# Performance work log

Measured on AMD Instinct MI355X. Metric: run time of the kernel, lower is better.

Reference implementation:

```python
import jax, jax.numpy as jnp
import numpy as np

VOCAB, EMB, NDIM, B, T = 50000, 300, 512, 128, 128


def gru_cell(x, h, Wih, Whh, bih, bhh):
    # torch nn.GRU gate order: [r, z, n]
    gi = x @ Wih.T + bih
    gh = h @ Whh.T + bhh
    i_r, i_z, i_n = jnp.split(gi, 3, axis=-1)
    h_r, h_z, h_n = jnp.split(gh, 3, axis=-1)
    r = jax.nn.sigmoid(i_r + h_r)
    z = jax.nn.sigmoid(i_z + h_z)
    n = jnp.tanh(i_n + r * h_n)
    return (1.0 - z) * n + z * h


def masked_gru(X, mask, h0, Wih, Whh, bih, bhh):
    # X: T x B x d, mask: T x B, h0: B x n. Replicates _gru_forward:
    # step-0 output is stored UNmasked (o_tm1 is None), later steps blend.
    h_raw = gru_cell(X[0], h0, Wih, Whh, bih, bhh)
    m0 = mask[0][:, None]
    h = h_raw * m0 + h0 * (1.0 - m0)
    o = h_raw

    def step(carry, inp):
        h, o = carry
        x_t, m_t = inp
        m = m_t[:, None]
        hr = gru_cell(x_t, h, Wih, Whh, bih, bhh)
        h_new = hr * m + h * (1.0 - m)
        o_new = hr * m + o * (1.0 - m)
        return (h_new, o_new), o_new

    (h_f, _), o_rest = jax.lax.scan(step, (h, o), (X[1:], mask[1:]))
    return jnp.concatenate([o[None], o_rest], axis=0), h_f


def rte_forward(premise, hypothesis, E, p_Wih, p_Whh, p_bih, p_bhh,
                h_Wih, h_Whh, h_bih, h_bhh, m_Wih, m_Whh, m_bih, m_bhh,
                W_y, W_h, W_r, W_alpha, out_W, out_b):
    bsz = premise.shape[0]
    n_dim = W_y.shape[0]
    mask_p = (premise != 0).astype(E.dtype).T            # T x B
    mask_h = (hypothesis != 0).astype(E.dtype).T
    enc_p = E[premise].transpose(1, 0, 2)                # T x B x EMB (eval: no dropout)
    enc_h = E[hypothesis].transpose(1, 0, 2)
    h0 = jnp.zeros((bsz, n_dim), dtype=E.dtype)
    o_p, h_n = masked_gru(enc_p, mask_p, h0, p_Wih, p_Whh, p_bih, p_bhh)
    o_h, _ = masked_gru(enc_h, mask_h, h_n, h_Wih, h_Whh, h_bih, h_bhh)

    Y = o_p.transpose(1, 0, 2)                           # B x Tp x n
    Yw = Y @ W_y                                         # hoisted: constant across steps
    maskY = mask_p.T                                     # B x Tp

    def step(r, inp):
        h_t, m_t = inp
        s = h_t @ W_h + r @ W_r                          # B x n
        M = jnp.tanh(Yw + s[:, None, :])                 # B x Tp x n
        alpha = (M @ W_alpha)[..., 0]                    # B x Tp
        alpha = alpha - 1000.0 * (1.0 - maskY)
        alpha = jax.nn.softmax(alpha, axis=-1)
        a = jnp.einsum('bt,btn->bn', alpha, Y)
        m_in = jnp.concatenate([a, h_t], axis=-1)        # B x 2n
        rr = gru_cell(m_in, r, m_Wih, m_Whh, m_bih, m_bhh)
        m = m_t[:, None]
        r_new = rr * m + r * (1.0 - m)
        return r_new, alpha

    r0 = jnp.zeros((bsz, n_dim), dtype=E.dtype)
    r_f, _alpha_vec = jax.lax.scan(step, r0, (o_h, mask_h))
    logits = r_f @ out_W.T + out_b                       # B x 3
    return jax.nn.log_softmax(logits, axis=-1)


def setup_inputs():
    key = jax.random.key(0)
    ks = jax.random.split(key, 22)
    s = 0.05
    def rn(k, sh):
        return jax.random.normal(k, sh, dtype=jnp.float32) * s
    G = 3 * NDIM
    return {
        "premise": jax.random.randint(ks[0], (B, T), 0, VOCAB),
        "hypothesis": jax.random.randint(ks[1], (B, T), 0, VOCAB),
        "E": rn(ks[2], (VOCAB, EMB)),
        "p_Wih": rn(ks[3], (G, EMB)), "p_Whh": rn(ks[4], (G, NDIM)),
        "p_bih": rn(ks[5], (G,)), "p_bhh": rn(ks[6], (G,)),
        "h_Wih": rn(ks[7], (G, EMB)), "h_Whh": rn(ks[8], (G, NDIM)),
        "h_bih": rn(ks[9], (G,)), "h_bhh": rn(ks[10], (G,)),
        "m_Wih": rn(ks[11], (G, 2 * NDIM)), "m_Whh": rn(ks[12], (G, NDIM)),
        "m_bih": rn(ks[13], (G,)), "m_bhh": rn(ks[14], (G,)),
        "W_y": rn(ks[15], (NDIM, NDIM)), "W_h": rn(ks[16], (NDIM, NDIM)),
        "W_r": rn(ks[17], (NDIM, NDIM)), "W_alpha": rn(ks[18], (NDIM, 1)),
        "out_W": rn(ks[19], (3, NDIM)), "out_b": rn(ks[20], (3,)),
    }


def reference(premise, hypothesis, E, p_Wih, p_Whh, p_bih, p_bhh,
              h_Wih, h_Whh, h_bih, h_bhh, m_Wih, m_Whh, m_bih, m_bhh,
              W_y, W_h, W_r, W_alpha, out_W, out_b):
    return rte_forward(premise, hypothesis, E, p_Wih, p_Whh, p_bih, p_bhh,
                       h_Wih, h_Whh, h_bih, h_bhh, m_Wih, m_Whh, m_bih, m_bhh,
                       W_y, W_h, W_r, W_alpha, out_W, out_b)
```

## Files before the change

kernel.cpp:

```cpp
#include <hip/hip_runtime.h>
#include <math.h>

#define B_SZ 128
#define T_SZ 128
#define EMBD 300
#define ND 512
#define G3 1536
#define FPAD 32
#define NFID 128
#define NREP 8

typedef short s16x8 __attribute__((ext_vector_type(8)));
typedef float f32x4 __attribute__((ext_vector_type(4)));
typedef unsigned long long u64;

__device__ __forceinline__ unsigned short f2b(float x) {
    unsigned u = __float_as_uint(x);
    unsigned r = (u + 0x7fff + ((u >> 16) & 1)) >> 16;
    return (unsigned short)r;
}
__device__ __forceinline__ float b2f(unsigned short v) {
    return __uint_as_float(((unsigned)v) << 16);
}
__device__ __forceinline__ unsigned pk2(float lo, float hi) {
    return (unsigned)f2b(lo) | ((unsigned)f2b(hi) << 16);
}
__device__ __forceinline__ float fsigmoid(float x) { return 1.0f / (1.0f + __expf(-x)); }
__device__ __forceinline__ float ftanh(float x) { return 1.0f - 2.0f / (__expf(2.0f * x) + 1.0f); }

__device__ __forceinline__ float dot2bf(unsigned a, unsigned b, float c) {
    asm("v_dot2_f32_bf16 %0, %1, %2, %0" : "+v"(c) : "v"(a), "v"(b));
    return c;
}

__device__ __forceinline__ f32x4 mfma16(s16x8 a, s16x8 b, f32x4 c) {
    return __builtin_amdgcn_mfma_f32_16x16x32_bf16(a, b, c, 0, 0, 0);
}

__device__ __forceinline__ u64 cld64(const void* p) {
    return __hip_atomic_load((const u64*)p, __ATOMIC_RELAXED, __HIP_MEMORY_SCOPE_AGENT);
}
__device__ __forceinline__ void cst64(void* p, u64 v) {
    __hip_atomic_store((u64*)p, v, __ATOMIC_RELAXED, __HIP_MEMORY_SCOPE_AGENT);
}
__device__ __forceinline__ unsigned cld32(const void* p) {
    return __hip_atomic_load((const unsigned*)p, __ATOMIC_RELAXED, __HIP_MEMORY_SCOPE_AGENT);
}
__device__ __forceinline__ void cst32(void* p, unsigned v) {
    __hip_atomic_store((unsigned*)p, v, __ATOMIC_RELAXED, __HIP_MEMORY_SCOPE_AGENT);
}
__device__ __forceinline__ s16x8 cld_frag(const unsigned short* p) {
    union { u64 q[2]; s16x8 v; } u;
    u.q[0] = cld64(p);
    u.q[1] = cld64(p + 4);
    return u.v;
}

__device__ __forceinline__ void postflag(unsigned* flags, int base, int id, unsigned ep)
{
    if (threadIdx.x < NREP)
        cst32(&flags[((long)threadIdx.x * NFID + base + id) * FPAD], ep);
}
__device__ __forceinline__ void waitflags(const unsigned* flags, int base, int n,
                                          unsigned ep, int rep)
{
    const unsigned* fr = flags + (long)rep * NFID * FPAD;
    if (threadIdx.x < 64) {
#pragma unroll 1
        for (int i = threadIdx.x; i < n; i += 64)
            while (cld32(&fr[(long)(base + i) * FPAD]) < ep)
                __builtin_amdgcn_s_sleep(2);
    }
    __syncthreads();
}
__device__ __forceinline__ void fbar(unsigned* flags, int base, int nb, unsigned ep)
{
    __syncthreads();
    postflag(flags, base, blockIdx.x & 63, ep);
    waitflags(flags, base, nb, ep, blockIdx.x & 7);
}

#define FB_GRUP 0
#define FB_GRUH 64

template<typename AT, bool OB>
__global__ __launch_bounds__(256)
void mfma_gemm(const AT* __restrict__ A, const int* __restrict__ idxA,
               const unsigned short* __restrict__ Wb, const float* __restrict__ bias,
               void* __restrict__ Cv,
               int M, int N, int K, int ldA, int Kpad, int ldC)
{
    __shared__ unsigned short As[64][40];
    __shared__ unsigned short Bs[64][40];
    const int tid = threadIdx.x;
    const int wv = tid >> 6, lane = tid & 63;
    const int wm = wv >> 1, wn = wv & 1;
    const int m0 = blockIdx.y * 64, n0 = blockIdx.x * 64;

    f32x4 acc[2][2] = {{{0.f,0.f,0.f,0.f},{0.f,0.f,0.f,0.f}},
                       {{0.f,0.f,0.f,0.f},{0.f,0.f,0.f,0.f}}};
    const int r_st = tid >> 2, k_st = (tid & 3) * 8;

    long arow = -1;
    {
        int gm = m0 + r_st;
        if (gm < M) arow = idxA ? (long)idxA[gm] : (long)gm;
    }

    const int kIters = (K + 31) / 32;
    for (int it = 0; it < kIters; ++it) {
        const int kg = it * 32 + k_st;
        {
            s16x8 pk = {0,0,0,0,0,0,0,0};
            if (arow >= 0) {
                if constexpr (sizeof(AT) == 2) {
                    if (kg + 8 <= K) {
                        pk = *(const s16x8*)((const unsigned short*)A + arow * (long)ldA + kg);
                    } else {
#pragma unroll
                        for (int j = 0; j < 8; ++j)
                            if (kg + j < K) pk[j] = (short)((const unsigned short*)A)[arow * (long)ldA + kg + j];
                    }
                } else {
                    if (kg + 8 <= K) {
                        const float* p = (const float*)A + arow * (long)ldA + kg;
                        f32x4 u0 = *(const f32x4*)p;
                        f32x4 u1 = *(const f32x4*)(p + 4);
#pragma unroll
                        for (int j = 0; j < 4; ++j) { pk[j] = (short)f2b(u0[j]); pk[4+j] = (short)f2b(u1[j]); }
                    } else {
#pragma unroll
                        for (int j = 0; j < 8; ++j) {
                            int kk = kg + j;
                            if (kk < K) pk[j] = (short)f2b(((const float*)A)[arow * (long)ldA + kk]);
                        }
                    }
                }
            }
            *(s16x8*)&As[r_st][k_st] = pk;
        }
        {
            int gn = n0 + r_st;
            s16x8 pk = {0,0,0,0,0,0,0,0};
            if (gn < N) pk = *(const s16x8*)&Wb[(long)gn * Kpad + kg];
            *(s16x8*)&Bs[r_st][k_st] = pk;
        }
        __syncthreads();
        {
            const int koff = (lane >> 4) * 8;
            s16x8 af[2], bfr[2];
#pragma unroll
            for (int f = 0; f < 2; ++f) {
                af[f]  = *(s16x8*)&As[wm * 32 + f * 16 + (lane & 15)][koff];
                bfr[f] = *(s16x8*)&Bs[wn * 32 + f * 16 + (lane & 15)][koff];
            }
#pragma unroll
            for (int fi = 0; fi < 2; ++fi)
#pragma unroll
                for (int fj = 0; fj < 2; ++fj)
                    acc[fi][fj] = mfma16(af[fi], bfr[fj], acc[fi][fj]);
        }
        __syncthreads();
    }
#pragma unroll
    for (int fi = 0; fi < 2; ++fi)
#pragma unroll
        for (int fj = 0; fj < 2; ++fj)
#pragma unroll
            for (int r = 0; r < 4; ++r) {
                int m = m0 + wm * 32 + fi * 16 + (lane >> 4) * 4 + r;
                int n = n0 + wn * 32 + fj * 16 + (lane & 15);
                if (m < M && n < N) {
                    float v = acc[fi][fj][r];
                    if (bias) v += bias[n];
                    if constexpr (OB) ((unsigned short*)Cv)[(long)m * ldC + n] = f2b(v);
                    else               ((float*)Cv)[(long)m * ldC + n] = v;
                }
            }
}

#define GRU_NB 64
__global__ __launch_bounds__(256, 1)
void gru_chain(const unsigned short* __restrict__ Whh_b, const float* __restrict__ GI,
               const float* __restrict__ bhh, const int* __restrict__ toks,
               float* __restrict__ h32,
               unsigned short* __restrict__ h16a, unsigned short* __restrict__ h16b,
               unsigned short* __restrict__ o_bt,
               unsigned* __restrict__ flags, int fbase)
{
    __shared__ unsigned short wlds[3][16][512];
    __shared__ unsigned short ht[64][20];
    const int tid = threadIdx.x;
    const int wv = tid >> 6, lane = tid & 63;
    const int dt = blockIdx.x & 31, bh = blockIdx.x >> 5;
    const int b0 = bh * 64;

    for (int s = 0; s < 12; ++s) {
        int slot = tid + s * 256;
        int g = slot >> 10, rem = slot & 1023, ks = rem >> 6, ln = rem & 63;
        int row = g * ND + dt * 16 + (ln & 15);
        int k = ks * 32 + (ln >> 4) * 8;
        *(s16x8*)&wlds[g][ks][ln * 8] = *(const s16x8*)&Whh_b[(long)row * ND + k];
    }
    __syncthreads();

    const int d = dt * 16 + (lane & 15);
    const int brow = b0 + wv * 16 + (lane >> 4) * 4;
    const long fhrd = ((long)(bh * 4 + wv) * 16) << 9;

    const int bl = tid & 63, dq = tid >> 6;
    const long fhwr = (((long)(bh * 4 + (bl >> 4)) * 16 + (dt >> 1)) << 9)
                    + (((((dt & 1) * 16 + dq * 4) >> 3) * 16 + (bl & 15)) * 8)
                    + (((dt & 1) * 16 + dq * 4) & 7);

    float hreg[4];
#pragma unroll
    for (int rr = 0; rr < 4; ++rr) hreg[rr] = h32[(long)(brow + rr) * ND + d];

    float o_run[4] = {0.f, 0.f, 0.f, 0.f};
    unsigned ep = 0;

    for (int t = 0; t < T_SZ; ++t) {
        const unsigned short* hin16 = (t & 1) ? h16b : h16a;
        unsigned short* hout16 = (t & 1) ? h16a : h16b;

        const float* git = GI + (long)t * (B_SZ * G3);
        float gi_r[4], gi_z[4], gi_n[4]; int mk[4];
#pragma unroll
        for (int rr = 0; rr < 4; ++rr) {
            int b = brow + rr;
            gi_r[rr] = git[(long)b * G3 + d];
            gi_z[rr] = git[(long)b * G3 + ND + d];
            gi_n[rr] = git[(long)b * G3 + 2 * ND + d];
            mk[rr]   = toks[b * T_SZ + t];
        }

        f32x4 acc0 = {0,0,0,0}, acc1 = {0,0,0,0}, acc2 = {0,0,0,0};
#pragma unroll
        for (int ks = 0; ks < 16; ++ks) {
            s16x8 a  = cld_frag(&hin16[fhrd + ((long)ks << 9) + lane * 8]);
            s16x8 br = *(s16x8*)&wlds[0][ks][lane * 8];
            s16x8 bz = *(s16x8*)&wlds[1][ks][lane * 8];
            s16x8 bn = *(s16x8*)&wlds[2][ks][lane * 8];
            acc0 = mfma16(a, br, acc0);
            acc1 = mfma16(a, bz, acc1);
            acc2 = mfma16(a, bn, acc2);
        }

#pragma unroll
        for (int rr = 0; rr < 4; ++rr) {
            int b = brow + rr;
            float rg = fsigmoid(gi_r[rr] + acc0[rr] + bhh[d]);
            float zg = fsigmoid(gi_z[rr] + acc1[rr] + bhh[ND + d]);
            float ng = ftanh(gi_n[rr] + rg * (acc2[rr] + bhh[2 * ND + d]));
            float hr = (1.0f - zg) * ng + zg * hreg[rr];
            bool m = mk[rr] != 0;
            float hn = m ? hr : hreg[rr];
            hreg[rr] = hn;
            ht[b - b0][lane & 15] = f2b(hn);
            if (t == T_SZ - 1) h32[(long)b * ND + d] = hn;
            o_run[rr] = (t == 0) ? hr : (m ? hr : o_run[rr]);
            o_bt[((long)b * T_SZ + t) * ND + d] = f2b(o_run[rr]);
        }
        __syncthreads();
        {
            u64 v = *(u64*)&ht[bl][dq * 4];
            cst64(&hout16[fhwr], v);
        }
        fbar(flags, fbase, GRU_NB, ++ep);
    }
}

__global__ __launch_bounds__(512, 1)
void match_pb(const unsigned short* __restrict__ Ws,
              const unsigned short* __restrict__ Wg,
              const unsigned short* __restrict__ OHWh_bt,
              const unsigned short* __restrict__ OHGI_bt,
              const float* __restrict__ m_bhh, const float* __restrict__ Walpha,
              const unsigned short* __restrict__ Yw_bb,
              const unsigned short* __restrict__ Y_bb,
              const int* __restrict__ prem, const int* __restrict__ hyp,
              float* __restrict__ r32)
{
    __shared__ unsigned ytp[64][512];
    __shared__ float sarr[512];
    __shared__ float wal[512];
    __shared__ float part[512];
    __shared__ float lg[T_SZ];
    __shared__ unsigned lgp[64];
    __shared__ unsigned xa16[256];
    __shared__ unsigned xr16[256];
    __shared__ float xr32[512];

    const int b = blockIdx.x;
    const int tid = threadIdx.x;
    const int tp = tid >> 2, q = tid & 3;

    for (int s = 0; s < 8; ++s) {
        int idx = s * 512 + tid;
        int rp = idx >> 6, n0 = (idx & 63) * 8;
        s16x8 y0 = *(const s16x8*)&Y_bb[((long)b * T_SZ + 2 * rp) * ND + n0];
        s16x8 y1 = *(const s16x8*)&Y_bb[((long)b * T_SZ + 2 * rp + 1) * ND + n0];
#pragma unroll
        for (int j = 0; j < 8; ++j)
            ytp[rp][n0 + j] = (unsigned)(unsigned short)y0[j]
                            | ((unsigned)(unsigned short)y1[j] << 16);
    }
    s16x8 ywr[16];
#pragma unroll
    for (int i8 = 0; i8 < 16; ++i8)
        ywr[i8] = *(const s16x8*)&Yw_bb[((long)b * T_SZ + tp) * ND + q * 128 + i8 * 8];

    wal[tid] = Walpha[tid];
    xr32[tid] = 0.0f;
    if (tid < 256) xr16[tid] = 0u;
    float mm = 0.f;
    if (tid < T_SZ) mm = (prem[b * T_SZ + tid] != 0) ? 0.f : 1000.f;
    __syncthreads();

    const float* sp  = &sarr[q * 128];
    const float* wap = &wal[q * 128];
    const unsigned* wsp = (const unsigned*)Ws + tid * 4;
    const unsigned* wgp = (const unsigned*)Wg + tid * 4;
    const unsigned ONE2 = 0x3F803F80u;

    for (int t = 0; t < T_SZ; ++t) {
        {
            float acc = 0.f;
#pragma unroll 4
            for (int k8 = 0; k8 < 64; ++k8) {
                unsigned x0 = xr16[k8 * 4], x1 = xr16[k8 * 4 + 1];
                unsigned x2 = xr16[k8 * 4 + 2], x3 = xr16[k8 * 4 + 3];
                const unsigned* w = wsp + (long)k8 * 2048;
                acc = dot2bf(w[0], x0, acc);
                acc = dot2bf(w[1], x1, acc);
                acc = dot2bf(w[2], x2, acc);
                acc = dot2bf(w[3], x3, acc);
            }
            sarr[tid] = acc + b2f(OHWh_bt[((long)b * T_SZ + t) * ND + tid]);
        }
        __syncthreads();
        {
            float acc = 0.f;
#pragma unroll
            for (int i8 = 0; i8 < 16; ++i8) {
                s16x8 yw = ywr[i8];
                f32x4 s0 = *(const f32x4*)&sp[i8 * 8];
                f32x4 s1 = *(const f32x4*)&sp[i8 * 8 + 4];
                f32x4 w0 = *(const f32x4*)&wap[i8 * 8];
                f32x4 w1 = *(const f32x4*)&wap[i8 * 8 + 4];
#pragma unroll
                for (int j = 0; j < 4; ++j)
                    acc += ftanh(b2f((unsigned short)yw[j]) + s0[j]) * w0[j];
#pragma unroll
                for (int j = 0; j < 4; ++j)
                    acc += ftanh(b2f((unsigned short)yw[4 + j]) + s1[j]) * w1[j];
            }
            part[tid] = acc;
        }
        __syncthreads();
        if (tid < T_SZ)
            lg[tid] = __expf(part[tid * 4] + part[tid * 4 + 1]
                           + part[tid * 4 + 2] + part[tid * 4 + 3] - mm);
        __syncthreads();
        if (tid < 64) lgp[tid] = pk2(lg[2 * tid], lg[2 * tid + 1]);
        __syncthreads();
        {
            float av = 0.f, su = 0.f;
#pragma unroll 8
            for (int i = 0; i < 64; ++i) {
                unsigned l2 = lgp[i];
                unsigned y2 = ytp[i][tid];
                av = dot2bf(l2, y2, av);
                su = dot2bf(l2, ONE2, su);
            }
            part[tid] = av / su;
        }
        __syncthreads();
        if (tid < 256) xa16[tid] = pk2(part[2 * tid], part[2 * tid + 1]);
        __syncthreads();
        {
            float aR = 0.f, aZ = 0.f, aGN = 0.f, aHN = 0.f;
#pragma unroll 2
            for (int k8 = 0; k8 < 64; ++k8) {
                unsigned xa0 = xa16[k8 * 4], xa1 = xa16[k8 * 4 + 1];
                unsigned xa2 = xa16[k8 * 4 + 2], xa3 = xa16[k8 * 4 + 3];
                unsigned xr0 = xr16[k8 * 4], xr1 = xr16[k8 * 4 + 1];
                unsigned xr2 = xr16[k8 * 4 + 2], xr3 = xr16[k8 * 4 + 3];
                const unsigned* w0 = wgp + (long)k8 * 2048;
                const unsigned* w1 = w0 + (1L << 17);
                const unsigned* w2 = w0 + (2L << 17);
                const unsigned* w3 = w0 + (3L << 17);
                const unsigned* w4 = w0 + (4L << 17);
                const unsigned* w5 = w0 + (5L << 17);
                aR  = dot2bf(w0[0], xa0, aR);  aR  = dot2bf(w0[1], xa1, aR);
                aR  = dot2bf(w0[2], xa2, aR);  aR  = dot2bf(w0[3], xa3, aR);
                aZ  = dot2bf(w1[0], xa0, aZ);  aZ  = dot2bf(w1[1], xa1, aZ);
                aZ  = dot2bf(w1[2], xa2, aZ);  aZ  = dot2bf(w1[3], xa3, aZ);
                aGN = dot2bf(w2[0], xa0, aGN); aGN = dot2bf(w2[1], xa1, aGN);
                aGN = dot2bf(w2[2], xa2, aGN); aGN = dot2bf(w2[3], xa3, aGN);
                aR  = dot2bf(w3[0], xr0, aR);  aR  = dot2bf(w3[1], xr1, aR);
                aR  = dot2bf(w3[2], xr2, aR);  aR  = dot2bf(w3[3], xr3, aR);
                aZ  = dot2bf(w4[0], xr0, aZ);  aZ  = dot2bf(w4[1], xr1, aZ);
                aZ  = dot2bf(w4[2], xr2, aZ);  aZ  = dot2bf(w4[3], xr3, aZ);
                aHN = dot2bf(w5[0], xr0, aHN); aHN = dot2bf(w5[1], xr1, aHN);
                aHN = dot2bf(w5[2], xr2, aHN); aHN = dot2bf(w5[3], xr3, aHN);
            }
            const unsigned short* og = OHGI_bt + ((long)b * T_SZ + t) * G3;
            float rg = fsigmoid(aR + b2f(og[tid]) + m_bhh[tid]);
            float zg = fsigmoid(aZ + b2f(og[ND + tid]) + m_bhh[ND + tid]);
            float ng = ftanh(aGN + b2f(og[2 * ND + tid])
                             + rg * (aHN + m_bhh[2 * ND + tid]));
            float rp = xr32[tid];
            float rn = (1.0f - zg) * ng + zg * rp;
            bool mk = hyp[b * T_SZ + t] != 0;
            float v = mk ? rn : rp;
            __syncthreads();
            xr32[tid] = v;
            part[tid] = v;
        }
        __syncthreads();
        if (tid < 256) xr16[tid] = pk2(part[2 * tid], part[2 * tid + 1]);
        __syncthreads();
    }
    r32[(long)b * ND + tid] = xr32[tid];
}

__global__ void prep_idx(const int* __restrict__ prem, const int* __restrict__ hyp,
                         int* __restrict__ idx_p, int* __restrict__ idx_h)
{
    int i = blockIdx.x * blockDim.x + threadIdx.x;
    if (i < B_SZ * T_SZ) {
        int t = i / B_SZ, b = i % B_SZ;
        idx_p[i] = prem[b * T_SZ + t];
        idx_h[i] = hyp[b * T_SZ + t];
    }
}

__global__ void conv_w(const float* __restrict__ in, unsigned short* __restrict__ out,
                       int N, int K, int Kpad, int ldIn, int colOff)
{
    long i = (long)blockIdx.x * blockDim.x + threadIdx.x;
    if (i >= (long)N * Kpad) return;
    int n = (int)(i / Kpad), k = (int)(i % Kpad);
    float v = (k < K) ? in[(long)n * ldIn + k + colOff] : 0.0f;
    out[i] = f2b(v);
}

__global__ void conv_wT(const float* __restrict__ in, unsigned short* __restrict__ out,
                        int N, int K, int Kpad, int ldIn)
{
    long i = (long)blockIdx.x * blockDim.x + threadIdx.x;
    if (i >= (long)N * Kpad) return;
    int n = (int)(i / Kpad), k = (int)(i % Kpad);
    float v = (k < K) ? in[(long)k * ldIn + n] : 0.0f;
    out[i] = f2b(v);
}

__global__ void pack_ws(const float* __restrict__ Wr, unsigned short* __restrict__ out)
{
    long i = (long)blockIdx.x * blockDim.x + threadIdx.x;
    if (i >= 64L * 512 * 8) return;
    int k8 = (int)(i >> 12), n = (int)((i >> 3) & 511), j = (int)(i & 7);
    out[i] = f2b(Wr[(long)(k8 * 8 + j) * ND + n]);
}

__global__ void pack_wg(const float* __restrict__ mWih, const float* __restrict__ mWhh,
                        unsigned short* __restrict__ out)
{
    long i = (long)blockIdx.x * blockDim.x + threadIdx.x;
    if (i >= 6L * 64 * 512 * 8) return;
    int fam = (int)(i >> 18);
    long rem = i & 262143;
    int k8 = (int)(rem >> 12), n = (int)((rem >> 3) & 511), j = (int)(rem & 7);
    int k = k8 * 8 + j;
    float v;
    if (fam < 3) v = mWih[(long)(fam * ND + n) * 1024 + k];
    else         v = mWhh[(long)((fam - 3) * ND + n) * ND + k];
    out[i] = f2b(v);
}

__global__ void zero_kernel(float* __restrict__ p, int n)
{
    int i = blockIdx.x * blockDim.x + threadIdx.x;
    if (i < n) p[i] = 0.0f;
}

__global__ void final_logits(const float* __restrict__ r, const float* __restrict__ outW,
                             const float* __restrict__ outb, float* __restrict__ out)
{
    int b = blockIdx.x;
    int lane = threadIdx.x;
    float a0 = 0.0f, a1 = 0.0f, a2 = 0.0f;
    for (int k = lane; k < ND; k += 64) {
        float rv = r[(long)b * ND + k];
        a0 += rv * outW[0 * ND + k];
        a1 += rv * outW[1 * ND + k];
        a2 += rv * outW[2 * ND + k];
    }
#pragma unroll
    for (int off = 32; off; off >>= 1) {
        a0 += __shfl_down(a0, off);
        a1 += __shfl_down(a1, off);
        a2 += __shfl_down(a2, off);
    }
    if (lane == 0) {
        float l0 = a0 + outb[0], l1 = a1 + outb[1], l2 = a2 + outb[2];
        float mx = fmaxf(l0, fmaxf(l1, l2));
        float se = expf(l0 - mx) + expf(l1 - mx) + expf(l2 - mx);
        float ls = mx + logf(se);
        out[b * 3 + 0] = l0 - ls;
        out[b * 3 + 1] = l1 - ls;
        out[b * 3 + 2] = l2 - ls;
    }
}

extern "C" void kernel_launch(void* const* d_in, const int* in_sizes, int n_in,
                              void* d_out, int out_size, void* d_ws, size_t ws_size,
                              hipStream_t stream)
{
    const int*   prem    = (const int*)d_in[0];
    const int*   hyp     = (const int*)d_in[1];
    const float* E       = (const float*)d_in[2];
    const float* p_Wih   = (const float*)d_in[3];
    const float* p_Whh   = (const float*)d_in[4];
    const float* p_bih   = (const float*)d_in[5];
    const float* p_bhh   = (const float*)d_in[6];
    const float* h_Wih   = (const float*)d_in[7];
    const float* h_Whh   = (const float*)d_in[8];
    const float* h_bih   = (const float*)d_in[9];
    const float* h_bhh   = (const float*)d_in[10];
    const float* m_Wih   = (const float*)d_in[11];
    const float* m_Whh   = (const float*)d_in[12];
    const float* m_bih   = (const float*)d_in[13];
    const float* m_bhh   = (const float*)d_in[14];
    const float* W_y     = (const float*)d_in[15];
    const float* W_h     = (const float*)d_in[16];
    const float* W_r     = (const float*)d_in[17];
    const float* W_alpha = (const float*)d_in[18];
    const float* out_W   = (const float*)d_in[19];
    const float* out_b   = (const float*)d_in[20];
    float* out = (float*)d_out;

    const int MB = T_SZ * B_SZ;
    const int NFLAGS = NREP * NFID * FPAD;

    float* ws = (float*)d_ws;
    size_t off = 0;
    float* GI    = ws + off; off += (size_t)MB * G3;
    float* h32   = ws + off; off += (size_t)B_SZ * ND;
    float* r32   = ws + off; off += (size_t)B_SZ * ND;
    unsigned* flags = (unsigned*)(ws + off); off += NFLAGS;
    int* idx_p = (int*)(ws + off); off += (size_t)B_SZ * T_SZ;
    int* idx_h = (int*)(ws + off); off += (size_t)B_SZ * T_SZ;
    unsigned short* ub = (unsigned short*)(ws + off);
    size_t uoff = 0;
    unsigned short* o_p_bt = ub + uoff; uoff += (size_t)MB * ND;
    unsigned short* o_h_bt = ub + uoff; uoff += (size_t)MB * ND;
    unsigned short* Yw_bb  = ub + uoff; uoff += (size_t)MB * ND;
    unsigned short* OHWh_bt= ub + uoff; uoff += (size_t)MB * ND;
    unsigned short* OHGI_bt= ub + uoff; uoff += (size_t)MB * G3;
    unsigned short* h16a   = ub + uoff; uoff += (size_t)B_SZ * ND;
    unsigned short* h16b   = ub + uoff; uoff += (size_t)B_SZ * ND;
    unsigned short* pWih_b = ub + uoff; uoff += (size_t)G3 * 320;
    unsigned short* hWih_b = ub + uoff; uoff += (size_t)G3 * 320;
    unsigned short* pWhh_b = ub + uoff; uoff += (size_t)G3 * ND;
    unsigned short* hWhh_b = ub + uoff; uoff += (size_t)G3 * ND;
    unsigned short* mWihR  = ub + uoff; uoff += (size_t)G3 * ND;
    unsigned short* WyT_b  = ub + uoff; uoff += (size_t)ND * ND;
    unsigned short* WhT_b  = ub + uoff; uoff += (size_t)ND * ND;
    unsigned short* Ws_p   = ub + uoff; uoff += 64L * 512 * 8;
    unsigned short* Wg_p   = ub + uoff; uoff += 6L * 64 * 512 * 8;
    off += (uoff + 1) / 2;
    if (ws_size < off * sizeof(float)) return;

    auto cblk = [](long n) { return (int)((n + 255) / 256); };

    prep_idx<<<cblk(MB), 256, 0, stream>>>(prem, hyp, idx_p, idx_h);
    conv_w <<<cblk((long)G3 * 320), 256, 0, stream>>>(p_Wih, pWih_b, G3, EMBD, 320, EMBD, 0);
    conv_w <<<cblk((long)G3 * 320), 256, 0, stream>>>(h_Wih, hWih_b, G3, EMBD, 320, EMBD, 0);
    conv_w <<<cblk((long)G3 * ND), 256, 0, stream>>>(p_Whh, pWhh_b, G3, ND, ND, ND, 0);
    conv_w <<<cblk((long)G3 * ND), 256, 0, stream>>>(h_Whh, hWhh_b, G3, ND, ND, ND, 0);
    conv_w <<<cblk((long)G3 * ND), 256, 0, stream>>>(m_Wih, mWihR, G3, ND, ND, 2 * ND, ND);
    conv_wT<<<cblk((long)ND * ND), 256, 0, stream>>>(W_y, WyT_b, ND, ND, ND, ND);
    conv_wT<<<cblk((long)ND * ND), 256, 0, stream>>>(W_h, WhT_b, ND, ND, ND, ND);
    pack_ws<<<cblk(64L * 512 * 8), 256, 0, stream>>>(W_r, Ws_p);
    pack_wg<<<cblk(6L * 64 * 512 * 8), 256, 0, stream>>>(m_Wih, m_Whh, Wg_p);
    zero_kernel<<<cblk(B_SZ * ND), 256, 0, stream>>>(h32, B_SZ * ND);
    zero_kernel<<<cblk(B_SZ * ND / 2), 256, 0, stream>>>((float*)h16a, B_SZ * ND / 2);
    zero_kernel<<<cblk(NFLAGS), 256, 0, stream>>>((float*)flags, NFLAGS);

    {
        dim3 g(G3 / 64, MB / 64);
        mfma_gemm<float, false><<<g, 256, 0, stream>>>(E, idx_p, pWih_b, p_bih, GI,
                                                       MB, G3, EMBD, EMBD, 320, G3);
    }
    gru_chain<<<GRU_NB, 256, 0, stream>>>(pWhh_b, GI, p_bhh, prem, h32, h16a, h16b,
                                          o_p_bt, flags, FB_GRUP);

    {
        dim3 g(G3 / 64, MB / 64);
        mfma_gemm<float, false><<<g, 256, 0, stream>>>(E, idx_h, hWih_b, h_bih, GI,
                                                       MB, G3, EMBD, EMBD, 320, G3);
    }
    gru_chain<<<GRU_NB, 256, 0, stream>>>(hWhh_b, GI, h_bhh, hyp, h32, h16a, h16b,
                                          o_h_bt, flags, FB_GRUH);

    {
        dim3 g(ND / 64, MB / 64);
        mfma_gemm<unsigned short, true><<<g, 256, 0, stream>>>(o_p_bt, nullptr, WyT_b, nullptr,
                                                               Yw_bb, MB, ND, ND, ND, ND, ND);
        mfma_gemm<unsigned short, true><<<g, 256, 0, stream>>>(o_h_bt, nullptr, WhT_b, nullptr,
                                                               OHWh_bt, MB, ND, ND, ND, ND, ND);
        dim3 g2(G3 / 64, MB / 64);
        mfma_gemm<unsigned short, true><<<g2, 256, 0, stream>>>(o_h_bt, nullptr, mWihR, m_bih,
                                                                OHGI_bt, MB, G3, ND, ND, ND, G3);
    }

    match_pb<<<B_SZ, 512, 0, stream>>>(Ws_p, Wg_p, OHWh_bt, OHGI_bt, m_bhh, W_alpha,
                                       Yw_bb, o_p_bt, prem, hyp, r32);

    final_logits<<<B_SZ, 64, 0, stream>>>(r32, out_W, out_b, out);
}
```

Measured before the change: 7.502 ms.

## Double match_pb block to 1024 threads, splitting dot products across two halves

The attention-matching recurrent kernel now runs 1024 threads per batch block instead of 512. The W_r matvec and the attention-weighted sum over Y are split along K into two halves and reduced through shared memory. The GRU gate matvec is split by gate pairs, with each half computing either R/GN or Z/HN. This roughly halves the serial per-thread work at each of the 128 sequential steps, at the cost of extra barriers, shared-memory reductions and higher register pressure under the 1024-thread launch bound.

```diff
diff --git a/kernel.cpp b/kernel.cpp
--- a/kernel.cpp
+++ b/kernel.cpp
@@ -271,7 +271,7 @@
     }
 }
 
-__global__ __launch_bounds__(512, 1)
+__global__ __launch_bounds__(1024, 1)
 void match_pb(const unsigned short* __restrict__ Ws,
               const unsigned short* __restrict__ Wg,
               const unsigned short* __restrict__ OHWh_bt,
@@ -285,19 +285,21 @@
     __shared__ unsigned ytp[64][512];
     __shared__ float sarr[512];
     __shared__ float wal[512];
-    __shared__ float part[512];
-    __shared__ float lg[T_SZ];
+    __shared__ float part[1024];
     __shared__ unsigned lgp[64];
-    __shared__ unsigned xa16[256];
-    __shared__ unsigned xr16[256];
+    __shared__ float red[2];
+    __shared__ float gR[512], gZ[512], gGN[512], gHN[512];
+    __shared__ unsigned short xa16h[512];
+    __shared__ unsigned short xr16h[512];
     __shared__ float xr32[512];
 
     const int b = blockIdx.x;
     const int tid = threadIdx.x;
-    const int tp = tid >> 2, q = tid & 3;
-
-    for (int s = 0; s < 8; ++s) {
-        int idx = s * 512 + tid;
+    const int nn = tid & 511, hh = tid >> 9;
+    const int tp = tid & 127, qq = tid >> 7;
+
+    for (int s = 0; s < 4; ++s) {
+        int idx = s * 1024 + tid;
         int rp = idx >> 6, n0 = (idx & 63) * 8;
         s16x8 y0 = *(const s16x8*)&Y_bb[((long)b * T_SZ + 2 * rp) * ND + n0];
         s16x8 y1 = *(const s16x8*)&Y_bb[((long)b * T_SZ + 2 * rp + 1) * ND + n0];
@@ -306,44 +308,53 @@
             ytp[rp][n0 + j] = (unsigned)(unsigned short)y0[j]
                             | ((unsigned)(unsigned short)y1[j] << 16);
     }
-    s16x8 ywr[16];
-#pragma unroll
-    for (int i8 = 0; i8 < 16; ++i8)
-        ywr[i8] = *(const s16x8*)&Yw_bb[((long)b * T_SZ + tp) * ND + q * 128 + i8 * 8];
-
-    wal[tid] = Walpha[tid];
-    xr32[tid] = 0.0f;
-    if (tid < 256) xr16[tid] = 0u;
-    float mm = 0.f;
-    if (tid < T_SZ) mm = (prem[b * T_SZ + tid] != 0) ? 0.f : 1000.f;
+    s16x8 ywr[8];
+#pragma unroll
+    for (int i8 = 0; i8 < 8; ++i8)
+        ywr[i8] = *(const s16x8*)&Yw_bb[((long)b * T_SZ + tp) * ND + qq * 64 + i8 * 8];
+
+    if (tid < 512) {
+        wal[tid] = Walpha[tid];
+        xr32[tid] = 0.0f;
+        xr16h[tid] = 0;
+    }
+    float mm0 = 0.f, mm1 = 0.f;
+    if (tid < 64) {
+        mm0 = (prem[b * T_SZ + 2 * tid] != 0) ? 0.f : 1000.f;
+        mm1 = (prem[b * T_SZ + 2 * tid + 1] != 0) ? 0.f : 1000.f;
+    }
     __syncthreads();
 
-    const float* sp  = &sarr[q * 128];
-    const float* wap = &wal[q * 128];
-    const unsigned* wsp = (const unsigned*)Ws + tid * 4;
-    const unsigned* wgp = (const unsigned*)Wg + tid * 4;
+    const unsigned* xaU = (const unsigned*)xa16h;
+    const unsigned* xrU = (const unsigned*)xr16h;
     const unsigned ONE2 = 0x3F803F80u;
 
     for (int t = 0; t < T_SZ; ++t) {
         {
             float acc = 0.f;
+            const unsigned* w = (const unsigned*)Ws + nn * 4 + (long)hh * 32 * 2048;
+            const unsigned* xr = xrU + hh * 128;
 #pragma unroll 4
-            for (int k8 = 0; k8 < 64; ++k8) {
-                unsigned x0 = xr16[k8 * 4], x1 = xr16[k8 * 4 + 1];
-                unsigned x2 = xr16[k8 * 4 + 2], x3 = xr16[k8 * 4 + 3];
-                const unsigned* w = wsp + (long)k8 * 2048;
-                acc = dot2bf(w[0], x0, acc);
-                acc = dot2bf(w[1], x1, acc);
-                acc = dot2bf(w[2], x2, acc);
-                acc = dot2bf(w[3], x3, acc);
-            }
-            sarr[tid] = acc + b2f(OHWh_bt[((long)b * T_SZ + t) * ND + tid]);
-        }
+            for (int k8 = 0; k8 < 32; ++k8) {
+                const unsigned* wk = w + (long)k8 * 2048;
+                acc = dot2bf(wk[0], xr[k8 * 4], acc);
+                acc = dot2bf(wk[1], xr[k8 * 4 + 1], acc);
+                acc = dot2bf(wk[2], xr[k8 * 4 + 2], acc);
+                acc = dot2bf(wk[3], xr[k8 * 4 + 3], acc);
+            }
+            part[tid] = acc;
+        }
+        __syncthreads();
+        if (tid < 512)
+            sarr[tid] = part[tid] + part[512 + tid]
+                      + b2f(OHWh_bt[((long)b * T_SZ + t) * ND + tid]);
         __syncthreads();
         {
             float acc = 0.f;
-#pragma unroll
-            for (int i8 = 0; i8 < 16; ++i8) {
+            const float* sp  = &sarr[qq * 64];
+            const float* wap = &wal[qq * 64];
+#pragma unroll
+            for (int i8 = 0; i8 < 8; ++i8) {
                 s16x8 yw = ywr[i8];
                 f32x4 s0 = *(const f32x4*)&sp[i8 * 8];
                 f32x4 s1 = *(const f32x4*)&sp[i8 * 8 + 4];
@@ -359,71 +370,81 @@
             part[tid] = acc;
         }
         __syncthreads();
-        if (tid < T_SZ)
-            lg[tid] = __expf(part[tid * 4] + part[tid * 4 + 1]
-                           + part[tid * 4 + 2] + part[tid * 4 + 3] - mm);
-        __syncthreads();
-        if (tid < 64) lgp[tid] = pk2(lg[2 * tid], lg[2 * tid + 1]);
+        if (tid < 64) {
+            float l0 = 0.f, l1 = 0.f;
+#pragma unroll
+            for (int q2 = 0; q2 < 8; ++q2) {
+                l0 += part[q2 * 128 + 2 * tid];
+                l1 += part[q2 * 128 + 2 * tid + 1];
+            }
+            lgp[tid] = pk2(__expf(l0 - mm0), __expf(l1 - mm1));
+        }
         __syncthreads();
         {
             float av = 0.f, su = 0.f;
+            const int i0 = hh * 32;
 #pragma unroll 8
-            for (int i = 0; i < 64; ++i) {
-                unsigned l2 = lgp[i];
-                unsigned y2 = ytp[i][tid];
-                av = dot2bf(l2, y2, av);
-                su = dot2bf(l2, ONE2, su);
-            }
-            part[tid] = av / su;
-        }
-        __syncthreads();
-        if (tid < 256) xa16[tid] = pk2(part[2 * tid], part[2 * tid + 1]);
-        __syncthreads();
-        {
-            float aR = 0.f, aZ = 0.f, aGN = 0.f, aHN = 0.f;
+            for (int i = 0; i < 32; ++i) {
+                unsigned l2 = lgp[i0 + i];
+                av = dot2bf(l2, ytp[i0 + i][nn], av);
+                if (nn == 0) su = dot2bf(l2, ONE2, su);
+            }
+            part[tid] = av;
+            if (nn == 0) red[hh] = su;
+        }
+        __syncthreads();
+        if (tid < 512) {
+            float inv = 1.0f / (red[0] + red[1]);
+            xa16h[tid] = f2b((part[tid] + part[512 + tid]) * inv);
+        }
+        __syncthreads();
+        {
+            const int d = nn, g2 = hh;
+            const unsigned* wbase = (const unsigned*)Wg + d * 4;
+            const unsigned* wA = wbase + ((long)(g2 ? 1 : 0) << 17);
+            const unsigned* wB = wbase + ((long)(g2 ? 4 : 3) << 17);
+            const unsigned* wC = wbase + ((long)(g2 ? 5 : 2) << 17);
+            const unsigned* xC = g2 ? xrU : xaU;
+            float acc1 = 0.f, acc2 = 0.f;
 #pragma unroll 2
             for (int k8 = 0; k8 < 64; ++k8) {
-                unsigned xa0 = xa16[k8 * 4], xa1 = xa16[k8 * 4 + 1];
-                unsigned xa2 = xa16[k8 * 4 + 2], xa3 = xa16[k8 * 4 + 3];
-                unsigned xr0 = xr16[k8 * 4], xr1 = xr16[k8 * 4 + 1];
-                unsigned xr2 = xr16[k8 * 4 + 2], xr3 = xr16[k8 * 4 + 3];
-                const unsigned* w0 = wgp + (long)k8 * 2048;
-                const unsigned* w1 = w0 + (1L << 17);
-                const unsigned* w2 = w0 + (2L << 17);
-                const unsigned* w3 = w0 + (3L << 17);
-                const unsigned* w4 = w0 + (4L << 17);
-                const unsigned* w5 = w0 + (5L << 17);
-                aR  = dot2bf(w0[0], xa0, aR);  aR  = dot2bf(w0[1], xa1, aR);
-                aR  = dot2bf(w0[2], xa2, aR);  aR  = dot2bf(w0[3], xa3, aR);
-                aZ  = dot2bf(w1[0], xa0, aZ);  aZ  = dot2bf(w1[1], xa1, aZ);
-                aZ  = dot2bf(w1[2], xa2, aZ);  aZ  = dot2bf(w1[3], xa3, aZ);
-                aGN = dot2bf(w2[0], xa0, aGN); aGN = dot2bf(w2[1], xa1, aGN);
-                aGN = dot2bf(w2[2], xa2, aGN); aGN = dot2bf(w2[3], xa3, aGN);
-                aR  = dot2bf(w3[0], xr0, aR);  aR  = dot2bf(w3[1], xr1, aR);
-                aR  = dot2bf(w3[2], xr2, aR);  aR  = dot2bf(w3[3], xr3, aR);
-                aZ  = dot2bf(w4[0], xr0, aZ);  aZ  = dot2bf(w4[1], xr1, aZ);
-                aZ  = dot2bf(w4[2], xr2, aZ);  aZ  = dot2bf(w4[3], xr3, aZ);
-                aHN = dot2bf(w5[0], xr0, aHN); aHN = dot2bf(w5[1], xr1, aHN);
-                aHN = dot2bf(w5[2], xr2, aHN); aHN = dot2bf(w5[3], xr3, aHN);
-            }
+                const long ko = (long)k8 * 2048;
+                unsigned xa0 = xaU[k8 * 4],     xa1 = xaU[k8 * 4 + 1];
+                unsigned xa2 = xaU[k8 * 4 + 2], xa3 = xaU[k8 * 4 + 3];
+                unsigned xr0 = xrU[k8 * 4],     xr1 = xrU[k8 * 4 + 1];
+                unsigned xr2 = xrU[k8 * 4 + 2], xr3 = xrU[k8 * 4 + 3];
+                unsigned xc0 = g2 ? xr0 : xa0,  xc1 = g2 ? xr1 : xa1;
+                unsigned xc2 = g2 ? xr2 : xa2,  xc3 = g2 ? xr3 : xa3;
+                const unsigned* a = wA + ko;
+                const unsigned* r = wB + ko;
+                const unsigned* c = wC + ko;
+                acc1 = dot2bf(a[0], xa0, acc1); acc1 = dot2bf(a[1], xa1, acc1);
+                acc1 = dot2bf(a[2], xa2, acc1); acc1 = dot2bf(a[3], xa3, acc1);
+                acc1 = dot2bf(r[0], xr0, acc1); acc1 = dot2bf(r[1], xr1, acc1);
+                acc1 = dot2bf(r[2], xr2, acc1); acc1 = dot2bf(r[3], xr3, acc1);
+                acc2 = dot2bf(c[0], xc0, acc2); acc2 = dot2bf(c[1], xc1, acc2);
+                acc2 = dot2bf(c[2], xc2, acc2); acc2 = dot2bf(c[3], xc3, acc2);
+            }
+            if (g2 == 0) { gR[d] = acc1; gGN[d] = acc2; }
+            else         { gZ[d] = acc1; gHN[d] = acc2; }
+        }
+        __syncthreads();
+        if (tid < 512) {
             const unsigned short* og = OHGI_bt + ((long)b * T_SZ + t) * G3;
-            float rg = fsigmoid(aR + b2f(og[tid]) + m_bhh[tid]);
-            float zg = fsigmoid(aZ + b2f(og[ND + tid]) + m_bhh[ND + tid]);
-            float ng = ftanh(aGN + b2f(og[2 * ND + tid])
-                             + rg * (aHN + m_bhh[2 * ND + tid]));
+            float rg = fsigmoid(gR[tid] + b2f(og[tid]) + m_bhh[tid]);
+            float zg = fsigmoid(gZ[tid] + b2f(og[ND + tid]) + m_bhh[ND + tid]);
+            float ng = ftanh(gGN[tid] + b2f(og[2 * ND + tid])
+                             + rg * (gHN[tid] + m_bhh[2 * ND + tid]));
             float rp = xr32[tid];
             float rn = (1.0f - zg) * ng + zg * rp;
             bool mk = hyp[b * T_SZ + t] != 0;
             float v = mk ? rn : rp;
-            __syncthreads();
             xr32[tid] = v;
-            part[tid] = v;
-        }
-        __syncthreads();
-        if (tid < 256) xr16[tid] = pk2(part[2 * tid], part[2 * tid + 1]);
-        __syncthreads();
-    }
-    r32[(long)b * ND + tid] = xr32[tid];
+            xr16h[tid] = f2b(v);
+        }
+        __syncthreads();
+    }
+    if (tid < 512) r32[(long)b * ND + tid] = xr32[tid];
 }
 
 __global__ void prep_idx(const int* __restrict__ prem, const int* __restrict__ hyp,
@@ -617,8 +638,8 @@
                                                                 OHGI_bt, MB, G3, ND, ND, ND, G3);
     }
 
-    match_pb<<<B_SZ, 512, 0, stream>>>(Ws_p, Wg_p, OHWh_bt, OHGI_bt, m_bhh, W_alpha,
-                                       Yw_bb, o_p_bt, prem, hyp, r32);
+    match_pb<<<B_SZ, 1024, 0, stream>>>(Ws_p, Wg_p, OHWh_bt, OHGI_bt, m_bhh, W_alpha,
+                                        Yw_bb, o_p_bt, prem, hyp, r32);
 
     final_logits<<<B_SZ, 64, 0, stream>>>(r32, out_W, out_b, out);
 }
```

Result: slower. 9.727 ms (+29.7%).
